# Optimization experiments

Measured on AMD Instinct MI355X. Metric: run time of the kernel, lower is better.

## Reference

```python
import jax, jax.numpy as jnp
import numpy as np

NUM_E = 200000   # number of entities/nodes
HID = 128        # hidsize
N_EDGES = 600000


def setup_inputs() -> dict:
    key = jax.random.key(0)
    k1, k2, k3, k4, k5, k6 = jax.random.split(key, 6)
    emb = jax.random.normal(k1, (NUM_E, HID), dtype=jnp.float32)
    edge_id = jax.random.randint(k2, (2, N_EDGES), 0, NUM_E, dtype=jnp.int64)
    edge_w = jax.random.uniform(k3, (N_EDGES,), dtype=jnp.float32)
    # MGCNConvLayer params (diag=True => diagonal/vector weights)
    w_diag = jax.random.normal(k4, (HID,), dtype=jnp.float32) * 0.1   # neighbor-path diag weight
    loop_w = jax.random.normal(k5, (HID,), dtype=jnp.float32) * 0.1   # jump/self-loop diag weight (isjump=True)
    bias = jnp.zeros((HID,), dtype=jnp.float32)
    res = jnp.asarray([0.1], dtype=jnp.float32)                       # StateHistory residual scale
    return {"emb": emb, "edge_id": edge_id, "edge_w": edge_w,
            "w_diag": w_diag, "loop_w": loop_w, "bias": bias, "res": res}


def reference(emb, edge_id, edge_w, w_diag, loop_w, bias, res):
    # --- MGCNConvLayer.forward(emb, edge_id, rel=None, num_e, dN=edge_w) ---
    src = edge_id[0]
    dst = edge_id[1]
    # gather source embeddings, weight by per-edge dN, scatter-add to destinations
    msg = emb[src] * edge_w[:, None]                       # [E, HID]
    agg = jax.ops.segment_sum(msg, dst, num_segments=NUM_E)  # [N, HID]
    # diagonal transform of aggregated messages + jump (self) path + bias, then act
    h = jnp.tanh(agg * w_diag + emb * loop_w + bias)        # [N, HID]
    # --- StateHistory tail: scaled residual; dropout is identity in eval ---
    tmp = res * h                                           # res broadcasts ([1])
    out = emb + tmp
    return (out, tmp)
```

## Files before the change

### kernel.cpp

```cpp
#include <hip/hip_runtime.h>

constexpr int NUM_E   = 200000;
constexpr int HID     = 128;
constexpr int N_EDGES = 600000;
constexpr int CAP     = 24;

typedef float    floatx4 __attribute__((ext_vector_type(4)));
typedef float    floatx8 __attribute__((ext_vector_type(8)));
typedef int      intx4   __attribute__((ext_vector_type(4)));
typedef _Float16 halfx4  __attribute__((ext_vector_type(4)));
typedef _Float16 halfx8  __attribute__((ext_vector_type(8)));


__global__ __launch_bounds__(256) void zero_cursor_kernel(int* __restrict__ cursor)
{
    int i = blockIdx.x * blockDim.x + threadIdx.x;
    if (i < NUM_E / 4) reinterpret_cast<intx4*>(cursor)[i] = (intx4)(0);
}

__global__ __launch_bounds__(256) void convert_zero_kernel(
    const float* __restrict__ emb, halfx8* __restrict__ embh8,
    int* __restrict__ cursor)
{
    int i = blockIdx.x * blockDim.x + threadIdx.x;
    constexpr int total = NUM_E * HID / 8;
    if (i < NUM_E / 4) reinterpret_cast<intx4*>(cursor)[i] = (intx4)(0);
    if (i >= total) return;
    const floatx4* e4 = reinterpret_cast<const floatx4*>(emb) + (size_t)i * 2;
    floatx4 v0 = __builtin_nontemporal_load(e4);
    floatx4 v1 = __builtin_nontemporal_load(e4 + 1);
    floatx8 v  = __builtin_shufflevector(v0, v1, 0, 1, 2, 3, 4, 5, 6, 7);
    embh8[i] = __builtin_convertvector(v, halfx8);
}

__global__ __launch_bounds__(256) void binning_kernel(
    const int* __restrict__ edge_id, const float* __restrict__ edge_w,
    int* __restrict__ cursor, int2* __restrict__ pairs)
{
    int e = blockIdx.x * blockDim.x + threadIdx.x;
    if (e < N_EDGES) {
        int d    = edge_id[N_EDGES + e];
        int slot = atomicAdd(&cursor[d], 1);
        if (slot < CAP)
            pairs[(size_t)d * CAP + slot] = make_int2(edge_id[e], __float_as_int(edge_w[e]));
    }
}

__global__ __launch_bounds__(256) void gather_epilogue_h_kernel(
    const halfx4* __restrict__ embh4,
    const int*    __restrict__ cursor,
    const int2*   __restrict__ pairs,
    const float*  __restrict__ w_diag,
    const float*  __restrict__ loop_w,
    const float*  __restrict__ bias,
    const float*  __restrict__ res,
    float*        __restrict__ out,
    float*        __restrict__ tmp)
{
    int t = blockIdx.x * blockDim.x + threadIdx.x;
    constexpr int total = NUM_E * 8;
    if (t >= total) return;
    int n = t >> 3;
    int c = t & 7;

    int deg = cursor[n];
    if (deg > CAP) deg = CAP;
    const int2* pb = pairs + (size_t)n * CAP;

    floatx4 a0 = (floatx4)(0.f);
    floatx4 a1 = (floatx4)(0.f);
    floatx4 a2 = (floatx4)(0.f);
    floatx4 a3 = (floatx4)(0.f);

    int k = 0;
    for (; k + 2 <= deg; k += 2) {
        int2 p0 = pb[k];
        int2 p1 = pb[k + 1];
        float w0 = __int_as_float(p0.y);
        float w1 = __int_as_float(p1.y);
        const halfx4* r0 = embh4 + (size_t)p0.x * (HID / 4);
        const halfx4* r1 = embh4 + (size_t)p1.x * (HID / 4);
        halfx4 h00 = r0[c], h01 = r0[c + 8], h02 = r0[c + 16], h03 = r0[c + 24];
        halfx4 h10 = r1[c], h11 = r1[c + 8], h12 = r1[c + 16], h13 = r1[c + 24];
        a0 += __builtin_convertvector(h00, floatx4) * w0;
        a1 += __builtin_convertvector(h01, floatx4) * w0;
        a2 += __builtin_convertvector(h02, floatx4) * w0;
        a3 += __builtin_convertvector(h03, floatx4) * w0;
        a0 += __builtin_convertvector(h10, floatx4) * w1;
        a1 += __builtin_convertvector(h11, floatx4) * w1;
        a2 += __builtin_convertvector(h12, floatx4) * w1;
        a3 += __builtin_convertvector(h13, floatx4) * w1;
    }
    if (k < deg) {
        int2 p0 = pb[k];
        float w0 = __int_as_float(p0.y);
        const halfx4* r0 = embh4 + (size_t)p0.x * (HID / 4);
        a0 += __builtin_convertvector(r0[c],      floatx4) * w0;
        a1 += __builtin_convertvector(r0[c + 8],  floatx4) * w0;
        a2 += __builtin_convertvector(r0[c + 16], floatx4) * w0;
        a3 += __builtin_convertvector(r0[c + 24], floatx4) * w0;
    }

    const float r = res[0];
    const halfx4* sr = embh4 + (size_t)n * (HID / 4);
    const floatx4* wd4 = reinterpret_cast<const floatx4*>(w_diag);
    const floatx4* lw4 = reinterpret_cast<const floatx4*>(loop_w);
    const floatx4* bb4 = reinterpret_cast<const floatx4*>(bias);
    floatx4* out4 = reinterpret_cast<floatx4*>(out);
    floatx4* tmp4 = reinterpret_cast<floatx4*>(tmp);
    const size_t base = (size_t)n * (HID / 4);

    floatx4 acc[4] = {a0, a1, a2, a3};
#pragma unroll
    for (int j = 0; j < 4; ++j) {
        int    cc  = c + 8 * j;
        size_t idx = base + cc;
        floatx4 ev = __builtin_convertvector(sr[cc], floatx4);
        floatx4 wd = wd4[cc], lw = lw4[cc], bb = bb4[cc];
        floatx4 tm, o;
        tm.x = r * tanhf(fmaf(acc[j].x, wd.x, fmaf(ev.x, lw.x, bb.x)));
        tm.y = r * tanhf(fmaf(acc[j].y, wd.y, fmaf(ev.y, lw.y, bb.y)));
        tm.z = r * tanhf(fmaf(acc[j].z, wd.z, fmaf(ev.z, lw.z, bb.z)));
        tm.w = r * tanhf(fmaf(acc[j].w, wd.w, fmaf(ev.w, lw.w, bb.w)));
        o = ev + tm;
        __builtin_nontemporal_store(o,  out4 + idx);
        __builtin_nontemporal_store(tm, tmp4 + idx);
    }
}

__global__ __launch_bounds__(256) void gather_epilogue_kernel(
    const float* __restrict__ emb,
    const int*   __restrict__ cursor,
    const int2*  __restrict__ pairs,
    const float* __restrict__ w_diag,
    const float* __restrict__ loop_w,
    const float* __restrict__ bias,
    const float* __restrict__ res,
    float*       __restrict__ out,
    float*       __restrict__ tmp)
{
    int t = blockIdx.x * blockDim.x + threadIdx.x;
    constexpr int total = NUM_E * 8;
    if (t >= total) return;
    int n = t >> 3;
    int c = t & 7;

    const floatx4* emb4 = reinterpret_cast<const floatx4*>(emb);
    int deg = cursor[n];
    if (deg > CAP) deg = CAP;
    const int2* pb = pairs + (size_t)n * CAP;

    floatx4 a0 = (floatx4)(0.f), a1 = (floatx4)(0.f);
    floatx4 a2 = (floatx4)(0.f), a3 = (floatx4)(0.f);

    int k = 0;
    for (; k + 2 <= deg; k += 2) {
        int2 p0 = pb[k], p1 = pb[k + 1];
        float w0 = __int_as_float(p0.y), w1 = __int_as_float(p1.y);
        const floatx4* r0 = emb4 + (size_t)p0.x * (HID / 4);
        const floatx4* r1 = emb4 + (size_t)p1.x * (HID / 4);
        a0 += r0[c] * w0;  a1 += r0[c + 8] * w0;  a2 += r0[c + 16] * w0;  a3 += r0[c + 24] * w0;
        a0 += r1[c] * w1;  a1 += r1[c + 8] * w1;  a2 += r1[c + 16] * w1;  a3 += r1[c + 24] * w1;
    }
    if (k < deg) {
        int2 p0 = pb[k];
        float w0 = __int_as_float(p0.y);
        const floatx4* r0 = emb4 + (size_t)p0.x * (HID / 4);
        a0 += r0[c] * w0;  a1 += r0[c + 8] * w0;  a2 += r0[c + 16] * w0;  a3 += r0[c + 24] * w0;
    }

    const float r = res[0];
    const floatx4* wd4 = reinterpret_cast<const floatx4*>(w_diag);
    const floatx4* lw4 = reinterpret_cast<const floatx4*>(loop_w);
    const floatx4* bb4 = reinterpret_cast<const floatx4*>(bias);
    floatx4* out4 = reinterpret_cast<floatx4*>(out);
    floatx4* tmp4 = reinterpret_cast<floatx4*>(tmp);
    const size_t base = (size_t)n * (HID / 4);

    floatx4 acc[4] = {a0, a1, a2, a3};
#pragma unroll
    for (int j = 0; j < 4; ++j) {
        int    cc  = c + 8 * j;
        size_t idx = base + cc;
        floatx4 ev = emb4[idx];
        floatx4 wd = wd4[cc], lw = lw4[cc], bb = bb4[cc];
        floatx4 tm, o;
        tm.x = r * tanhf(fmaf(acc[j].x, wd.x, fmaf(ev.x, lw.x, bb.x)));
        tm.y = r * tanhf(fmaf(acc[j].y, wd.y, fmaf(ev.y, lw.y, bb.y)));
        tm.z = r * tanhf(fmaf(acc[j].z, wd.z, fmaf(ev.z, lw.z, bb.z)));
        tm.w = r * tanhf(fmaf(acc[j].w, wd.w, fmaf(ev.w, lw.w, bb.w)));
        o = ev + tm;
        __builtin_nontemporal_store(o,  out4 + idx);
        __builtin_nontemporal_store(tm, tmp4 + idx);
    }
}

extern "C" void kernel_launch(void* const* d_in, const int* in_sizes, int n_in,
                              void* d_out, int out_size, void* d_ws, size_t ws_size,
                              hipStream_t stream) {
    const float* emb     = (const float*)d_in[0];
    const int*   edge_id = (const int*)  d_in[1];
    const float* edge_w  = (const float*)d_in[2];
    const float* w_diag  = (const float*)d_in[3];
    const float* loop_w  = (const float*)d_in[4];
    const float* bias    = (const float*)d_in[5];
    const float* res     = (const float*)d_in[6];

    float* out = (float*)d_out;
    float* tmp = out + (size_t)NUM_E * HID;

    int*    cursor = (int*)d_ws;
    int2*   pairs  = (int2*)(cursor + NUM_E);
    halfx8* embh8  = (halfx8*)(pairs + (size_t)NUM_E * CAP);
    halfx4* embh4  = (halfx4*)embh8;

    const size_t need_h = (size_t)NUM_E * 4 + (size_t)NUM_E * CAP * 8
                        + (size_t)NUM_E * HID * 2;

    if (ws_size >= need_h) {
        convert_zero_kernel<<<(NUM_E * HID / 8 + 255) / 256, 256, 0, stream>>>(
            emb, embh8, cursor);
        binning_kernel<<<(N_EDGES + 255) / 256, 256, 0, stream>>>(
            edge_id, edge_w, cursor, pairs);
        gather_epilogue_h_kernel<<<(NUM_E * 8 + 255) / 256, 256, 0, stream>>>(
            embh4, cursor, pairs, w_diag, loop_w, bias, res, out, tmp);
    } else {
        zero_cursor_kernel<<<(NUM_E / 4 + 255) / 256, 256, 0, stream>>>(cursor);
        binning_kernel<<<(N_EDGES + 255) / 256, 256, 0, stream>>>(
            edge_id, edge_w, cursor, pairs);
        gather_epilogue_kernel<<<(NUM_E * 8 + 255) / 256, 256, 0, stream>>>(
            emb, cursor, pairs, w_diag, loop_w, bias, res, out, tmp);
    }
}
```

Measured before the change: 126.8 us.

## Fuse edge binning into fp16 convert kernel and unroll first four gathers

Edge binning moves into the fp16 conversion kernel, so the binning atomics overlap with the bandwidth-bound convert pass. Cursor zeroing moves to a small separate kernel launched first. The gather loop now always issues the first four neighbor loads unconditionally, clamping the index and zeroing the weight when the node has fewer edges, to raise memory-level parallelism. The cost is redundant loads for low-degree nodes and a mix of atomic and streaming work in one kernel.

```diff
diff --git a/kernel.cpp b/kernel.cpp
--- a/kernel.cpp
+++ b/kernel.cpp
@@ -18,13 +18,23 @@
     if (i < NUM_E / 4) reinterpret_cast<intx4*>(cursor)[i] = (intx4)(0);
 }
 
-__global__ __launch_bounds__(256) void convert_zero_kernel(
+__global__ __launch_bounds__(256) void convert_bin_kernel(
     const float* __restrict__ emb, halfx8* __restrict__ embh8,
-    int* __restrict__ cursor)
+    const int* __restrict__ edge_id, const float* __restrict__ edge_w,
+    int* __restrict__ cursor, int2* __restrict__ pairs)
 {
     int i = blockIdx.x * blockDim.x + threadIdx.x;
     constexpr int total = NUM_E * HID / 8;
-    if (i < NUM_E / 4) reinterpret_cast<intx4*>(cursor)[i] = (intx4)(0);
+
+    if (i < N_EDGES) {
+        int s    = edge_id[i];
+        int d    = edge_id[N_EDGES + i];
+        float w  = edge_w[i];
+        int slot = atomicAdd(&cursor[d], 1);
+        if (slot < CAP)
+            pairs[(size_t)d * CAP + slot] = make_int2(s, __float_as_int(w));
+    }
+
     if (i >= total) return;
     const floatx4* e4 = reinterpret_cast<const floatx4*>(emb) + (size_t)i * 2;
     floatx4 v0 = __builtin_nontemporal_load(e4);
@@ -72,33 +82,28 @@
     floatx4 a2 = (floatx4)(0.f);
     floatx4 a3 = (floatx4)(0.f);
 
-    int k = 0;
-    for (; k + 2 <= deg; k += 2) {
-        int2 p0 = pb[k];
-        int2 p1 = pb[k + 1];
-        float w0 = __int_as_float(p0.y);
-        float w1 = __int_as_float(p1.y);
-        const halfx4* r0 = embh4 + (size_t)p0.x * (HID / 4);
-        const halfx4* r1 = embh4 + (size_t)p1.x * (HID / 4);
-        halfx4 h00 = r0[c], h01 = r0[c + 8], h02 = r0[c + 16], h03 = r0[c + 24];
-        halfx4 h10 = r1[c], h11 = r1[c + 8], h12 = r1[c + 16], h13 = r1[c + 24];
-        a0 += __builtin_convertvector(h00, floatx4) * w0;
-        a1 += __builtin_convertvector(h01, floatx4) * w0;
-        a2 += __builtin_convertvector(h02, floatx4) * w0;
-        a3 += __builtin_convertvector(h03, floatx4) * w0;
-        a0 += __builtin_convertvector(h10, floatx4) * w1;
-        a1 += __builtin_convertvector(h11, floatx4) * w1;
-        a2 += __builtin_convertvector(h12, floatx4) * w1;
-        a3 += __builtin_convertvector(h13, floatx4) * w1;
-    }
-    if (k < deg) {
-        int2 p0 = pb[k];
-        float w0 = __int_as_float(p0.y);
-        const halfx4* r0 = embh4 + (size_t)p0.x * (HID / 4);
-        a0 += __builtin_convertvector(r0[c],      floatx4) * w0;
-        a1 += __builtin_convertvector(r0[c + 8],  floatx4) * w0;
-        a2 += __builtin_convertvector(r0[c + 16], floatx4) * w0;
-        a3 += __builtin_convertvector(r0[c + 24], floatx4) * w0;
+    if (deg > 0) {
+        const int dm1 = deg - 1;
+#pragma unroll
+        for (int j = 0; j < 4; ++j) {
+            int  kk = (j < deg) ? j : dm1;
+            int2 p  = pb[kk];
+            float w = (j < deg) ? __int_as_float(p.y) : 0.f;
+            const halfx4* r0 = embh4 + (size_t)p.x * (HID / 4);
+            a0 += __builtin_convertvector(r0[c],      floatx4) * w;
+            a1 += __builtin_convertvector(r0[c + 8],  floatx4) * w;
+            a2 += __builtin_convertvector(r0[c + 16], floatx4) * w;
+            a3 += __builtin_convertvector(r0[c + 24], floatx4) * w;
+        }
+        for (int k = 4; k < deg; ++k) {
+            int2 p  = pb[k];
+            float w = __int_as_float(p.y);
+            const halfx4* r0 = embh4 + (size_t)p.x * (HID / 4);
+            a0 += __builtin_convertvector(r0[c],      floatx4) * w;
+            a1 += __builtin_convertvector(r0[c + 8],  floatx4) * w;
+            a2 += __builtin_convertvector(r0[c + 16], floatx4) * w;
+            a3 += __builtin_convertvector(r0[c + 24], floatx4) * w;
+        }
     }
 
     const float r = res[0];
@@ -218,10 +223,9 @@
                         + (size_t)NUM_E * HID * 2;
 
     if (ws_size >= need_h) {
-        convert_zero_kernel<<<(NUM_E * HID / 8 + 255) / 256, 256, 0, stream>>>(
-            emb, embh8, cursor);
-        binning_kernel<<<(N_EDGES + 255) / 256, 256, 0, stream>>>(
-            edge_id, edge_w, cursor, pairs);
+        zero_cursor_kernel<<<(NUM_E / 4 + 255) / 256, 256, 0, stream>>>(cursor);
+        convert_bin_kernel<<<(NUM_E * HID / 8 + 255) / 256, 256, 0, stream>>>(
+            emb, embh8, edge_id, edge_w, cursor, pairs);
         gather_epilogue_h_kernel<<<(NUM_E * 8 + 255) / 256, 256, 0, stream>>>(
             embh4, cursor, pairs, w_diag, loop_w, bias, res, out, tmp);
     } else {
```

Result: no change. 129.2 us (+1.8%).
